# Optimization experiments

Hardware: AMD Instinct MI355X
Metric: run time of the kernel (lower is better)

## Reference

```python
import jax, jax.numpy as jnp
import numpy as np

D_IN = 0.1
D_OUT = 1.0
LAMBDA_TC = 1.0
LAMBDA_OUT = 1.0
LAMBDA_CENT = 1.0


def setup_inputs() -> dict:
    key = jax.random.key(0)
    k1, k2, k3, k4, k5, k6 = jax.random.split(key, 6)
    B, D, C, L = 4096, 3072, 10, 128
    return {
        "x": jax.random.normal(k1, (B, D), jnp.float32),
        "x_hat": jax.random.normal(k2, (B, D), jnp.float32),
        "target": jax.random.randint(k3, (B,), 0, C, jnp.int32),
        "z_in": jax.random.normal(k4, (B, L), jnp.float32),
        "z_out": jax.random.normal(k5, (B, L), jnp.float32),
        "center_arr": jax.random.normal(k6, (C, L), jnp.float32),
    }


def _forward(x, x_hat, z_in, z_out, center_arr, target):
    # In-place no_grad row normalization of the center parameter in the original:
    # the param values are replaced by their normalized versions before use.
    norms = jax.lax.stop_gradient(jnp.linalg.norm(center_arr, axis=1, keepdims=True))
    centers = center_arr / norms  # [C, L]

    # mse reconstruction loss
    loss_mse = jnp.mean((x - x_hat) ** 2)

    # triplet-center loss, vectorized: pairwise L2 distances [B, C]
    diff = z_in[:, None, :] - centers[None, :, :]  # [B, C, L]
    dists = jnp.sqrt(jnp.sum(diff * diff, axis=-1))  # [B, C]
    B = z_in.shape[0]
    pos = dists[jnp.arange(B), target]  # distance to own-class center
    own = jax.nn.one_hot(target, centers.shape[0], dtype=jnp.bool_)  # [B, C]
    neg = jnp.min(jnp.where(own, jnp.inf, dists), axis=1)  # min over other classes
    loss_tc = jnp.mean(jnp.maximum(pos + D_IN - neg, 0.0))

    # outlier loss: push outlier latents outside radius d_out
    loss_out = jnp.mean(jnp.maximum(D_OUT - jnp.linalg.norm(z_out, axis=1), 0.0))

    # centroid orthogonality loss: || C C^T - I ||_F
    gram = centers @ centers.T  # [C, C]
    loss_orth = jnp.linalg.norm(gram - jnp.eye(gram.shape[0], dtype=gram.dtype))

    return loss_mse + LAMBDA_TC * loss_tc + LAMBDA_OUT * loss_out + LAMBDA_CENT * loss_orth


def reference(x, x_hat, target, z_in, z_out, center_arr):
    return _forward(x, x_hat, z_in, z_out, center_arr, target)
```

## Files before the change

### kernel.cpp

```cpp
#include <hip/hip_runtime.h>
#include <math.h>

#define D_IN_M      0.1f
#define D_OUT_M     1.0f
#define NBLK        256
#define NTHR        1024
#define NWAVE       16
#define SLOT_STRIDE 16

__device__ __forceinline__ float waveReduceSum(float v) {
    #pragma unroll
    for (int off = 32; off > 0; off >>= 1) v += __shfl_xor(v, off, 64);
    return v;
}

__global__ __launch_bounds__(NTHR, 4)
void cae_fused_kernel(const float4* __restrict__ x,
                      const float4* __restrict__ xh,
                      const int*    __restrict__ target,
                      const float*  __restrict__ z_in,
                      const float*  __restrict__ z_out,
                      const float*  __restrict__ center_arr,
                      float* __restrict__ ws,
                      unsigned* __restrict__ counter,
                      float* __restrict__ out,
                      long n4, int B, int C, int L,
                      float invBD, float invB) {
    extern __shared__ float smc[];
    __shared__ float sred[NWAVE];
    __shared__ float sorth;
    __shared__ unsigned is_last;

    const int tid  = threadIdx.x;
    const int wave = tid >> 6;
    const int lane = tid & 63;
    const int epl  = L >> 6;

    for (int c = wave; c < C; c += NWAVE) {
        const float e0 = center_arr[c * L + lane * epl + 0];
        const float e1 = center_arr[c * L + lane * epl + 1];
        const float ss = waveReduceSum(e0 * e0 + e1 * e1);
        const float inv = rsqrtf(ss);
        smc[c * L + lane * epl + 0] = e0 * inv;
        smc[c * L + lane * epl + 1] = e1 * inv;
    }
    if (tid == 0) sorth = 0.f;
    __syncthreads();

    float v = 0.f;

    {
        const long per_blk = n4 / gridDim.x;
        const long r0 = (long)blockIdx.x * per_blk;
        const long r1 = (blockIdx.x == gridDim.x - 1) ? n4 : r0 + per_blk;
        float acc = 0.f;
        long base = r0;
        for (; base + 6L * NTHR <= r1; base += 6L * NTHR) {
            const long i = base + tid;
            const float4 a0 = x[i];
            const float4 a1 = x[i + NTHR];
            const float4 a2 = x[i + 2 * NTHR];
            const float4 a3 = x[i + 3 * NTHR];
            const float4 a4 = x[i + 4 * NTHR];
            const float4 a5 = x[i + 5 * NTHR];
            const float4 b0 = xh[i];
            const float4 b1 = xh[i + NTHR];
            const float4 b2 = xh[i + 2 * NTHR];
            const float4 b3 = xh[i + 3 * NTHR];
            const float4 b4 = xh[i + 4 * NTHR];
            const float4 b5 = xh[i + 5 * NTHR];
            float d;
            d = a0.x - b0.x; acc += d * d; d = a0.y - b0.y; acc += d * d;
            d = a0.z - b0.z; acc += d * d; d = a0.w - b0.w; acc += d * d;
            d = a1.x - b1.x; acc += d * d; d = a1.y - b1.y; acc += d * d;
            d = a1.z - b1.z; acc += d * d; d = a1.w - b1.w; acc += d * d;
            d = a2.x - b2.x; acc += d * d; d = a2.y - b2.y; acc += d * d;
            d = a2.z - b2.z; acc += d * d; d = a2.w - b2.w; acc += d * d;
            d = a3.x - b3.x; acc += d * d; d = a3.y - b3.y; acc += d * d;
            d = a3.z - b3.z; acc += d * d; d = a3.w - b3.w; acc += d * d;
            d = a4.x - b4.x; acc += d * d; d = a4.y - b4.y; acc += d * d;
            d = a4.z - b4.z; acc += d * d; d = a4.w - b4.w; acc += d * d;
            d = a5.x - b5.x; acc += d * d; d = a5.y - b5.y; acc += d * d;
            d = a5.z - b5.z; acc += d * d; d = a5.w - b5.w; acc += d * d;
        }
        for (long j = base + tid; j < r1; j += NTHR) {
            const float4 a = x[j], b = xh[j];
            float d;
            d = a.x - b.x; acc += d * d; d = a.y - b.y; acc += d * d;
            d = a.z - b.z; acc += d * d; d = a.w - b.w; acc += d * d;
        }
        v = acc * invBD;
    }

    const int row = blockIdx.x * NWAVE + wave;
    if (row < B) {
        const float zi0 = z_in[row * L + lane * epl + 0];
        const float zi1 = z_in[row * L + lane * epl + 1];
        const int tgt = target[row];
        float pos = 0.f, neg = INFINITY;
        for (int c = 0; c < C; ++c) {
            const float d0 = zi0 - smc[c * L + lane * epl + 0];
            const float d1 = zi1 - smc[c * L + lane * epl + 1];
            const float d2 = waveReduceSum(d0 * d0 + d1 * d1);
            const float dist = sqrtf(d2);
            if (c == tgt) pos = dist;
            else          neg = fminf(neg, dist);
        }
        const float zo0 = z_out[row * L + lane * epl + 0];
        const float zo1 = z_out[row * L + lane * epl + 1];
        const float zo2 = waveReduceSum(zo0 * zo0 + zo1 * zo1);
        if (lane == 0) {
            const float tc = fmaxf(pos + D_IN_M - neg, 0.f);
            const float ol = fmaxf(D_OUT_M - sqrtf(zo2), 0.f);
            v += (tc + ol) * invB;
        }
    }

    if (blockIdx.x == 0) {
        float part = 0.f;
        for (int r = wave; r < C; r += NWAVE) {
            const float ra0 = smc[r * L + lane * epl + 0];
            const float ra1 = smc[r * L + lane * epl + 1];
            for (int cc = 0; cc < C; ++cc) {
                const float d = waveReduceSum(
                    ra0 * smc[cc * L + lane * epl + 0] +
                    ra1 * smc[cc * L + lane * epl + 1]);
                const float t = d - (cc == r ? 1.f : 0.f);
                part += t * t;
            }
        }
        if (lane == 0) atomicAdd(&sorth, part);
    }

    v = waveReduceSum(v);
    if (lane == 0) sred[wave] = v;
    __syncthreads();
    if (tid == 0) {
        float s = 0.f;
        #pragma unroll
        for (int w = 0; w < NWAVE; ++w) s += sred[w];
        if (blockIdx.x == 0) s += sqrtf(sorth);
        const float old = atomicExch(&ws[(long)blockIdx.x * SLOT_STRIDE], s);
        asm volatile("" :: "v"(old));
        const unsigned oc = atomicAdd(counter, 1u);
        is_last = (oc == NBLK - 1u) ? 1u : 0u;
    }
    __syncthreads();

    if (is_last) {
        float s = 0.f;
        for (int i = tid; i < NBLK; i += NTHR)
            s += atomicAdd(&ws[(long)i * SLOT_STRIDE], 0.0f);
        s = waveReduceSum(s);
        if (lane == 0) sred[wave] = s;
        __syncthreads();
        if (tid == 0) {
            float t = 0.f;
            #pragma unroll
            for (int w = 0; w < NWAVE; ++w) t += sred[w];
            out[0] = t;
        }
    }
}

extern "C" void kernel_launch(void* const* d_in, const int* in_sizes, int n_in,
                              void* d_out, int out_size, void* d_ws, size_t ws_size,
                              hipStream_t stream) {
    const float* x          = (const float*)d_in[0];
    const float* x_hat      = (const float*)d_in[1];
    const int*   target     = (const int*)d_in[2];
    const float* z_in       = (const float*)d_in[3];
    const float* z_out      = (const float*)d_in[4];
    const float* center_arr = (const float*)d_in[5];
    float* out = (float*)d_out;
    float* ws  = (float*)d_ws;

    const int B = in_sizes[2];
    const int D = in_sizes[0] / B;
    const int L = in_sizes[3] / B;
    const int C = in_sizes[5] / L;
    const long n4 = (long)B * D / 4;

    unsigned* counter = (unsigned*)(ws + (long)NBLK * SLOT_STRIDE);

    hipMemsetAsync(counter, 0, sizeof(unsigned), stream);

    cae_fused_kernel<<<NBLK, NTHR, C * L * sizeof(float), stream>>>(
        (const float4*)x, (const float4*)x_hat, target, z_in, z_out, center_arr,
        ws, counter, out, n4, B, C, L, 1.f / ((float)B * D), 1.f / (float)B);
}
```

Before: 32.56 us.

## Use many smaller blocks with grid-stride MSE and two-level completion counters

Switches from 256 blocks of 1024 threads to 2048 blocks of 256 threads, and turns the MSE streaming loop into a grid-stride loop over fixed 6-vector chunks per thread. The aim is to spread the bandwidth-bound reduction more evenly across CUs, raise occupancy, and give more memory parallelism. Only the first blocks that own latent rows now normalize the centers into shared memory. The single global completion counter becomes a two-level counter (per group of 64 blocks, then across groups) to reduce atomic contention. The trade-off is more blocks to launch and a final reduction that sums 2048 partial slots instead of 256.

```diff
diff --git a/kernel.cpp b/kernel.cpp
--- a/kernel.cpp
+++ b/kernel.cpp
@@ -3,10 +3,11 @@
 
 #define D_IN_M      0.1f
 #define D_OUT_M     1.0f
-#define NBLK        256
-#define NTHR        1024
-#define NWAVE       16
+#define NBLK        2048
+#define NTHR        256
 #define SLOT_STRIDE 16
+#define NGRP        32
+#define GRP_SZ      (NBLK / NGRP)
 
 __device__ __forceinline__ float waveReduceSum(float v) {
     #pragma unroll
@@ -14,7 +15,7 @@
     return v;
 }
 
-__global__ __launch_bounds__(NTHR, 4)
+__global__ __launch_bounds__(NTHR, 2)
 void cae_fused_kernel(const float4* __restrict__ x,
                       const float4* __restrict__ xh,
                       const int*    __restrict__ target,
@@ -22,12 +23,13 @@
                       const float*  __restrict__ z_out,
                       const float*  __restrict__ center_arr,
                       float* __restrict__ ws,
-                      unsigned* __restrict__ counter,
+                      unsigned* __restrict__ l1cnt,
+                      unsigned* __restrict__ l2cnt,
                       float* __restrict__ out,
                       long n4, int B, int C, int L,
                       float invBD, float invB) {
     extern __shared__ float smc[];
-    __shared__ float sred[NWAVE];
+    __shared__ float sred[4];
     __shared__ float sorth;
     __shared__ unsigned is_last;
 
@@ -35,64 +37,67 @@
     const int wave = tid >> 6;
     const int lane = tid & 63;
     const int epl  = L >> 6;
+    const long cpb = 6L * NTHR;
 
-    for (int c = wave; c < C; c += NWAVE) {
-        const float e0 = center_arr[c * L + lane * epl + 0];
-        const float e1 = center_arr[c * L + lane * epl + 1];
-        const float ss = waveReduceSum(e0 * e0 + e1 * e1);
-        const float inv = rsqrtf(ss);
-        smc[c * L + lane * epl + 0] = e0 * inv;
-        smc[c * L + lane * epl + 1] = e1 * inv;
+    const int nrowblk = (B + 3) >> 2;
+    if (blockIdx.x < (unsigned)nrowblk) {
+        for (int c = wave; c < C; c += 4) {
+            const float e0 = center_arr[c * L + lane * epl + 0];
+            const float e1 = center_arr[c * L + lane * epl + 1];
+            const float ss = waveReduceSum(e0 * e0 + e1 * e1);
+            const float inv = rsqrtf(ss);
+            smc[c * L + lane * epl + 0] = e0 * inv;
+            smc[c * L + lane * epl + 1] = e1 * inv;
+        }
+        if (tid == 0) sorth = 0.f;
+        __syncthreads();
     }
-    if (tid == 0) sorth = 0.f;
-    __syncthreads();
 
     float v = 0.f;
 
     {
-        const long per_blk = n4 / gridDim.x;
-        const long r0 = (long)blockIdx.x * per_blk;
-        const long r1 = (blockIdx.x == gridDim.x - 1) ? n4 : r0 + per_blk;
         float acc = 0.f;
-        long base = r0;
-        for (; base + 6L * NTHR <= r1; base += 6L * NTHR) {
-            const long i = base + tid;
-            const float4 a0 = x[i];
-            const float4 a1 = x[i + NTHR];
-            const float4 a2 = x[i + 2 * NTHR];
-            const float4 a3 = x[i + 3 * NTHR];
-            const float4 a4 = x[i + 4 * NTHR];
-            const float4 a5 = x[i + 5 * NTHR];
-            const float4 b0 = xh[i];
-            const float4 b1 = xh[i + NTHR];
-            const float4 b2 = xh[i + 2 * NTHR];
-            const float4 b3 = xh[i + 3 * NTHR];
-            const float4 b4 = xh[i + 4 * NTHR];
-            const float4 b5 = xh[i + 5 * NTHR];
-            float d;
-            d = a0.x - b0.x; acc += d * d; d = a0.y - b0.y; acc += d * d;
-            d = a0.z - b0.z; acc += d * d; d = a0.w - b0.w; acc += d * d;
-            d = a1.x - b1.x; acc += d * d; d = a1.y - b1.y; acc += d * d;
-            d = a1.z - b1.z; acc += d * d; d = a1.w - b1.w; acc += d * d;
-            d = a2.x - b2.x; acc += d * d; d = a2.y - b2.y; acc += d * d;
-            d = a2.z - b2.z; acc += d * d; d = a2.w - b2.w; acc += d * d;
-            d = a3.x - b3.x; acc += d * d; d = a3.y - b3.y; acc += d * d;
-            d = a3.z - b3.z; acc += d * d; d = a3.w - b3.w; acc += d * d;
-            d = a4.x - b4.x; acc += d * d; d = a4.y - b4.y; acc += d * d;
-            d = a4.z - b4.z; acc += d * d; d = a4.w - b4.w; acc += d * d;
-            d = a5.x - b5.x; acc += d * d; d = a5.y - b5.y; acc += d * d;
-            d = a5.z - b5.z; acc += d * d; d = a5.w - b5.w; acc += d * d;
-        }
-        for (long j = base + tid; j < r1; j += NTHR) {
-            const float4 a = x[j], b = xh[j];
-            float d;
-            d = a.x - b.x; acc += d * d; d = a.y - b.y; acc += d * d;
-            d = a.z - b.z; acc += d * d; d = a.w - b.w; acc += d * d;
+        for (long i0 = (long)blockIdx.x * cpb; i0 < n4; i0 += (long)gridDim.x * cpb) {
+            const long i = i0 + tid;
+            if (i0 + cpb <= n4) {
+                const float4 a0 = x[i];
+                const float4 a1 = x[i + NTHR];
+                const float4 a2 = x[i + 2 * NTHR];
+                const float4 a3 = x[i + 3 * NTHR];
+                const float4 a4 = x[i + 4 * NTHR];
+                const float4 a5 = x[i + 5 * NTHR];
+                const float4 b0 = xh[i];
+                const float4 b1 = xh[i + NTHR];
+                const float4 b2 = xh[i + 2 * NTHR];
+                const float4 b3 = xh[i + 3 * NTHR];
+                const float4 b4 = xh[i + 4 * NTHR];
+                const float4 b5 = xh[i + 5 * NTHR];
+                float d;
+                d = a0.x - b0.x; acc += d * d; d = a0.y - b0.y; acc += d * d;
+                d = a0.z - b0.z; acc += d * d; d = a0.w - b0.w; acc += d * d;
+                d = a1.x - b1.x; acc += d * d; d = a1.y - b1.y; acc += d * d;
+                d = a1.z - b1.z; acc += d * d; d = a1.w - b1.w; acc += d * d;
+                d = a2.x - b2.x; acc += d * d; d = a2.y - b2.y; acc += d * d;
+                d = a2.z - b2.z; acc += d * d; d = a2.w - b2.w; acc += d * d;
+                d = a3.x - b3.x; acc += d * d; d = a3.y - b3.y; acc += d * d;
+                d = a3.z - b3.z; acc += d * d; d = a3.w - b3.w; acc += d * d;
+                d = a4.x - b4.x; acc += d * d; d = a4.y - b4.y; acc += d * d;
+                d = a4.z - b4.z; acc += d * d; d = a4.w - b4.w; acc += d * d;
+                d = a5.x - b5.x; acc += d * d; d = a5.y - b5.y; acc += d * d;
+                d = a5.z - b5.z; acc += d * d; d = a5.w - b5.w; acc += d * d;
+            } else {
+                for (long j = i; j < n4; j += NTHR) {
+                    const float4 a = x[j], b = xh[j];
+                    float d;
+                    d = a.x - b.x; acc += d * d; d = a.y - b.y; acc += d * d;
+                    d = a.z - b.z; acc += d * d; d = a.w - b.w; acc += d * d;
+                }
+            }
         }
         v = acc * invBD;
     }
 
-    const int row = blockIdx.x * NWAVE + wave;
+    const int row = blockIdx.x * 4 + wave;
     if (row < B) {
         const float zi0 = z_in[row * L + lane * epl + 0];
         const float zi1 = z_in[row * L + lane * epl + 1];
@@ -118,7 +123,7 @@
 
     if (blockIdx.x == 0) {
         float part = 0.f;
-        for (int r = wave; r < C; r += NWAVE) {
+        for (int r = wave; r < C; r += 4) {
             const float ra0 = smc[r * L + lane * epl + 0];
             const float ra1 = smc[r * L + lane * epl + 1];
             for (int cc = 0; cc < C; ++cc) {
@@ -136,14 +141,17 @@
     if (lane == 0) sred[wave] = v;
     __syncthreads();
     if (tid == 0) {
-        float s = 0.f;
-        #pragma unroll
-        for (int w = 0; w < NWAVE; ++w) s += sred[w];
+        float s = sred[0] + sred[1] + sred[2] + sred[3];
         if (blockIdx.x == 0) s += sqrtf(sorth);
         const float old = atomicExch(&ws[(long)blockIdx.x * SLOT_STRIDE], s);
         asm volatile("" :: "v"(old));
-        const unsigned oc = atomicAdd(counter, 1u);
-        is_last = (oc == NBLK - 1u) ? 1u : 0u;
+        unsigned last = 0u;
+        const unsigned o1 = atomicAdd(&l1cnt[blockIdx.x >> 6], 1u);
+        if (o1 == GRP_SZ - 1u) {
+            const unsigned o2 = atomicAdd(l2cnt, 1u);
+            last = (o2 == NGRP - 1u) ? 1u : 0u;
+        }
+        is_last = last;
     }
     __syncthreads();
 
@@ -154,12 +162,7 @@
         s = waveReduceSum(s);
         if (lane == 0) sred[wave] = s;
         __syncthreads();
-        if (tid == 0) {
-            float t = 0.f;
-            #pragma unroll
-            for (int w = 0; w < NWAVE; ++w) t += sred[w];
-            out[0] = t;
-        }
+        if (tid == 0) out[0] = sred[0] + sred[1] + sred[2] + sred[3];
     }
 }
 
@@ -181,11 +184,12 @@
     const int C = in_sizes[5] / L;
     const long n4 = (long)B * D / 4;
 
-    unsigned* counter = (unsigned*)(ws + (long)NBLK * SLOT_STRIDE);
+    unsigned* l1cnt = (unsigned*)(ws + (long)NBLK * SLOT_STRIDE);
+    unsigned* l2cnt = l1cnt + NGRP;
 
-    hipMemsetAsync(counter, 0, sizeof(unsigned), stream);
+    hipMemsetAsync(l1cnt, 0, (NGRP + 1) * sizeof(unsigned), stream);
 
     cae_fused_kernel<<<NBLK, NTHR, C * L * sizeof(float), stream>>>(
         (const float4*)x, (const float4*)x_hat, target, z_in, z_out, center_arr,
-        ws, counter, out, n4, B, C, L, 1.f / ((float)B * D), 1.f / (float)B);
+        ws, l1cnt, l2cnt, out, n4, B, C, L, 1.f / ((float)B * D), 1.f / (float)B);
 }
```

Measured after the change: 44.22 us. +35.8%, slower.
